# Optimization experiments

Measured on AMD Instinct MI355X. Metric: run time of the kernel, lower is better.

## Reference

```python
import jax, jax.numpy as jnp
import numpy as np
from jax import lax


def setup_inputs() -> dict:
    key = jax.random.key(0)
    k1, k2 = jax.random.split(key)
    N, dim, m = 8192, 1024, 1024
    x = jax.random.normal(k1, (N, dim), dtype=jnp.float32)
    vectors = jax.random.normal(k2, (m, dim), dtype=jnp.float32) * 0.01
    bias = jnp.zeros((dim,), dtype=jnp.float32)
    return {"x": x, "vectors": vectors, "bias": bias}


def reference(x, vectors, bias):
    # Normalize each reflection vector to unit length: [m, d]
    v_normed = vectors / jnp.linalg.norm(vectors, axis=1, keepdims=True)

    def step(out, v):
        # out: [N, d], v: [d]
        proj = out @ v                       # [N]
        out = out - 2.0 * proj[:, None] * v  # rank-1 Householder update
        return out, None

    out, _ = lax.scan(step, x, v_normed)
    return out + bias
```

## Files before the change

### kernel.cpp

```cpp
#include <hip/hip_runtime.h>
#include <hip/hip_bf16.h>

typedef __attribute__((ext_vector_type(8))) short short8;
typedef __attribute__((ext_vector_type(4))) short s16x4;
typedef __attribute__((ext_vector_type(4))) float f32x4;

static __device__ inline short f2bf(float f) {
    unsigned u = __float_as_uint(f);
    unsigned r = (u + 0x7fffu + ((u >> 16) & 1u)) >> 16;
    return (short)r;
}
static __device__ inline float bf2f(short h) {
    return __uint_as_float(((unsigned)(unsigned short)h) << 16);
}

static __device__ inline int swz32(int row, int slot) {
    return row * 32 + ((slot ^ ((row >> 1) & 3)) << 3);
}
static __device__ inline int swz64(int row, int slot) {
    return row * 64 + ((slot ^ (row & 7)) << 3);
}

__global__ __launch_bounds__(256) void k_prep(const float* __restrict__ vec,
                                              short* __restrict__ Vh, short* __restrict__ Vl,
                                              short* __restrict__ Vth, short* __restrict__ Vtl,
                                              int m, int dim) {
    __shared__ float ps[32][9];
    __shared__ float invs[32];
    __shared__ float tile[32][33];
    int r0 = blockIdx.x * 32;
    int t = threadIdx.x;
    int r = t >> 3, seg = t & 7;
    const float* src = vec + (size_t)(r0 + r) * dim + seg * 128;
    float ss = 0.f;
#pragma unroll 8
    for (int i = 0; i < 32; ++i) {
        float4 v = *(const float4*)&src[i * 4];
        ss += v.x * v.x + v.y * v.y + v.z * v.z + v.w * v.w;
    }
    ps[r][seg] = ss;
    __syncthreads();
    if (t < 32) {
        float s = 0.f;
#pragma unroll
        for (int q = 0; q < 8; ++q) s += ps[t][q];
        invs[t] = 1.0f / sqrtf(s);
    }
    __syncthreads();
    float inv = invs[r];
    int c4 = (t & 7) * 4;
    for (int ct = 0; ct < dim / 32; ++ct) {
        float4 v = *(const float4*)&vec[(size_t)(r0 + r) * dim + ct * 32 + c4];
        float f[4] = {v.x * inv, v.y * inv, v.z * inv, v.w * inv};
        s16x4 h, l;
#pragma unroll
        for (int q = 0; q < 4; ++q) {
            h[q] = f2bf(f[q]);
            l[q] = f2bf(f[q] - bf2f(h[q]));
            tile[r][c4 + q] = f[q];
        }
        *(s16x4*)&Vh[(size_t)(r0 + r) * dim + ct * 32 + c4] = h;
        *(s16x4*)&Vl[(size_t)(r0 + r) * dim + ct * 32 + c4] = l;
        __syncthreads();
        s16x4 th, tl;
#pragma unroll
        for (int q = 0; q < 4; ++q) {
            float ff = tile[c4 + q][r];
            th[q] = f2bf(ff);
            tl[q] = f2bf(ff - bf2f(th[q]));
        }
        *(s16x4*)&Vth[(size_t)(ct * 32 + r) * m + r0 + c4] = th;
        *(s16x4*)&Vtl[(size_t)(ct * 32 + r) * m + r0 + c4] = tl;
        __syncthreads();
    }
}

__global__ __launch_bounds__(256) void k_cast(const float* __restrict__ X,
                                              short* __restrict__ Xh, int n4) {
    for (int i = blockIdx.x * blockDim.x + threadIdx.x; i < n4; i += gridDim.x * blockDim.x) {
        float4 v = ((const float4*)X)[i];
        float f[4] = {v.x, v.y, v.z, v.w};
        s16x4 h;
#pragma unroll
        for (int q = 0; q < 4; ++q) h[q] = f2bf(f[q]);
        *(s16x4*)&Xh[(size_t)i * 4] = h;
    }
}

template<int MODE, int TRI>
__global__ __launch_bounds__(256) void k_nt64g(
    const short* __restrict__ Ah, const short* __restrict__ Al,
    const short* __restrict__ Bh, const short* __restrict__ Bl,
    float* __restrict__ Cf, short* __restrict__ Ch, short* __restrict__ Cl,
    int K, int lda, int ldb, int ldc) {
    __shared__ short As[2][2][64 * 32];
    __shared__ short Bs[2][2][64 * 32];
    int i0 = blockIdx.y * 64, j0 = blockIdx.x * 64;
    if (TRI == 2 && j0 < i0) return;
    int KE = (TRI == 1) ? (j0 + 64) : K;
    int t = threadIdx.x, lane = t & 63, wave = t >> 6;
    int wr = wave >> 1, wc = wave & 1;
    int srow = wave * 16 + (lane >> 2);
    int sslot = (lane & 3) ^ ((lane >> 3) & 3);
    const short* gAh = &Ah[(size_t)(i0 + srow) * lda + sslot * 8];
    const short* gAl = &Al[(size_t)(i0 + srow) * lda + sslot * 8];
    const short* gBh = &Bh[(size_t)(j0 + srow) * ldb + sslot * 8];
    const short* gBl = &Bl[(size_t)(j0 + srow) * ldb + sslot * 8];
    auto stage = [&](int buf, int k0) {
        __builtin_amdgcn_global_load_lds((const __attribute__((address_space(1))) void*)&gAh[k0],
            (__attribute__((address_space(3))) void*)&As[buf][0][wave * 512], 16, 0, 0);
        __builtin_amdgcn_global_load_lds((const __attribute__((address_space(1))) void*)&gAl[k0],
            (__attribute__((address_space(3))) void*)&As[buf][1][wave * 512], 16, 0, 0);
        __builtin_amdgcn_global_load_lds((const __attribute__((address_space(1))) void*)&gBh[k0],
            (__attribute__((address_space(3))) void*)&Bs[buf][0][wave * 512], 16, 0, 0);
        __builtin_amdgcn_global_load_lds((const __attribute__((address_space(1))) void*)&gBl[k0],
            (__attribute__((address_space(3))) void*)&Bs[buf][1][wave * 512], 16, 0, 0);
    };
    int nIter = KE >> 5;
    stage(0, 0);
    f32x4 acc[2][2] = {};
    for (int it = 0; it < nIter; ++it) {
        int c = it & 1;
        if (it + 1 < nIter) {
            stage(c ^ 1, (it + 1) << 5);
            asm volatile("s_waitcnt vmcnt(4)" ::: "memory");
        } else {
            asm volatile("s_waitcnt vmcnt(0)" ::: "memory");
        }
        __builtin_amdgcn_s_barrier();
        __builtin_amdgcn_sched_barrier(0);
        int g = lane >> 4;
        short8 ah[2], al2[2], bh[2], bl2[2];
#pragma unroll
        for (int i = 0; i < 2; ++i) {
            int ro = swz32(wr * 32 + i * 16 + (lane & 15), g);
            ah[i] = *(const short8*)&As[c][0][ro];
            al2[i] = *(const short8*)&As[c][1][ro];
        }
#pragma unroll
        for (int j = 0; j < 2; ++j) {
            int ro = swz32(wc * 32 + j * 16 + (lane & 15), g);
            bh[j] = *(const short8*)&Bs[c][0][ro];
            bl2[j] = *(const short8*)&Bs[c][1][ro];
        }
#pragma unroll
        for (int i = 0; i < 2; ++i)
#pragma unroll
            for (int j = 0; j < 2; ++j) {
                acc[i][j] = __builtin_amdgcn_mfma_f32_16x16x32_bf16(ah[i], bh[j], acc[i][j], 0, 0, 0);
                acc[i][j] = __builtin_amdgcn_mfma_f32_16x16x32_bf16(ah[i], bl2[j], acc[i][j], 0, 0, 0);
                acc[i][j] = __builtin_amdgcn_mfma_f32_16x16x32_bf16(al2[i], bh[j], acc[i][j], 0, 0, 0);
            }
        asm volatile("s_waitcnt lgkmcnt(0)" ::: "memory");
        __builtin_amdgcn_s_barrier();
    }
#pragma unroll
    for (int i = 0; i < 2; ++i)
#pragma unroll
        for (int j = 0; j < 2; ++j) {
            int row0 = i0 + wr * 32 + i * 16 + ((lane >> 4) << 2);
            int col = j0 + wc * 32 + j * 16 + (lane & 15);
#pragma unroll
            for (int r = 0; r < 4; ++r) {
                float v = acc[i][j][r];
                size_t idx = (size_t)(row0 + r) * ldc + col;
                if (MODE == 2) {
                    Ch[idx] = f2bf((((row0 + r) == col) ? 1.f : 0.f) - v);
                } else {
                    short h = f2bf(v);
                    short l = f2bf(v - bf2f(h));
                    Ch[idx] = h;
                    Cl[idx] = l;
                    if (MODE == 3) Cf[idx] = v;
                }
            }
        }
}

__global__ __launch_bounds__(256) void k_baseinv2(const float* __restrict__ G,
                                                  short* __restrict__ Th, short* __restrict__ Tl,
                                                  short* __restrict__ Tth, short* __restrict__ Ttl,
                                                  int m) {
    __shared__ float Rs[64 * 64];
    int d = blockIdx.x >> 4, g = blockIdx.x & 15;
    int b0 = d * 64;
    int t = threadIdx.x, lane = t & 63, wave = t >> 6;
    {
        int r = t >> 2, c00 = (t & 3) * 16;
#pragma unroll
        for (int q = 0; q < 4; ++q)
            *(float4*)&Rs[r * 64 + c00 + q * 4] =
                *(const float4*)&G[(size_t)(b0 + r) * m + b0 + c00 + q * 4];
    }
    __syncthreads();
    int c = g * 4 + wave;
    float x = 0.f;
    for (int r = c; r >= 0; --r) {
        float prod = Rs[r * 64 + lane] * x;
        float s = prod;
#pragma unroll
        for (int off = 32; off; off >>= 1) s += __shfl_xor(s, off, 64);
        if (lane == r) x = ((r == c) ? 2.f : 0.f) - 2.f * s;
    }
    short h = f2bf(x);
    short l = f2bf(x - bf2f(h));
    Th[(size_t)(b0 + lane) * m + b0 + c] = h;
    Tl[(size_t)(b0 + lane) * m + b0 + c] = l;
    Tth[(size_t)(b0 + c) * m + b0 + lane] = h;
    Ttl[(size_t)(b0 + c) * m + b0 + lane] = l;
}

__global__ __launch_bounds__(256) void k_tree64f(const float* __restrict__ G,
                                                 short* __restrict__ Th, short* __restrict__ Tl,
                                                 short* __restrict__ Tth, short* __restrict__ Ttl,
                                                 int m) {
    __shared__ float Gb[64 * 65];
    __shared__ float Ai[64 * 65];
    __shared__ float Ci[64 * 64];
    __shared__ float Tm[64 * 64];
    int p = blockIdx.x;
    int a0 = p * 128, c0 = a0 + 64;
    int t = threadIdx.x;
    {
        int r = t >> 2, c00 = (t & 3) * 16;
#pragma unroll
        for (int q = 0; q < 4; ++q) {
            *(float4*)&Gb[r * 65 + c00 + q * 4] =
                *(const float4*)&G[(size_t)(a0 + r) * m + c0 + c00 + q * 4];
            s16x4 ha = *(const s16x4*)&Th[(size_t)(a0 + r) * m + a0 + c00 + q * 4];
            s16x4 la = *(const s16x4*)&Tl[(size_t)(a0 + r) * m + a0 + c00 + q * 4];
            s16x4 hc = *(const s16x4*)&Th[(size_t)(c0 + r) * m + c0 + c00 + q * 4];
            s16x4 lc = *(const s16x4*)&Tl[(size_t)(c0 + r) * m + c0 + c00 + q * 4];
#pragma unroll
            for (int e = 0; e < 4; ++e) {
                Ai[r * 65 + c00 + q * 4 + e] = bf2f(ha[e]) + bf2f(la[e]);
                Ci[r * 64 + c00 + q * 4 + e] = bf2f(hc[e]) + bf2f(lc[e]);
            }
        }
    }
    __syncthreads();
    int tx = t & 15, ty = t >> 4;
    float acc[4][4] = {};
#pragma unroll 4
    for (int k = 0; k < 64; ++k) {
        float av[4], bv[4];
#pragma unroll
        for (int i = 0; i < 4; ++i) av[i] = Gb[(ty * 4 + i) * 65 + k];
#pragma unroll
        for (int j = 0; j < 4; ++j) bv[j] = Ci[k * 64 + tx * 4 + j];
#pragma unroll
        for (int i = 0; i < 4; ++i)
#pragma unroll
            for (int j = 0; j < 4; ++j) acc[i][j] += av[i] * bv[j];
    }
#pragma unroll
    for (int i = 0; i < 4; ++i)
#pragma unroll
        for (int j = 0; j < 4; ++j) Tm[(ty * 4 + i) * 64 + tx * 4 + j] = acc[i][j];
    __syncthreads();
    float acc2[4][4] = {};
#pragma unroll 4
    for (int k = 0; k < 64; ++k) {
        float av[4], bv[4];
#pragma unroll
        for (int i = 0; i < 4; ++i) av[i] = Ai[(ty * 4 + i) * 65 + k];
#pragma unroll
        for (int j = 0; j < 4; ++j) bv[j] = Tm[k * 64 + tx * 4 + j];
#pragma unroll
        for (int i = 0; i < 4; ++i)
#pragma unroll
            for (int j = 0; j < 4; ++j) acc2[i][j] += av[i] * bv[j];
    }
#pragma unroll
    for (int i = 0; i < 4; ++i)
#pragma unroll
        for (int j = 0; j < 4; ++j) {
            float v = -acc2[i][j];
            short h = f2bf(v);
            short l = f2bf(v - bf2f(h));
            int R = a0 + ty * 4 + i, C = c0 + tx * 4 + j;
            Th[(size_t)R * m + C] = h;
            Tl[(size_t)R * m + C] = l;
            Tth[(size_t)C * m + R] = h;
            Ttl[(size_t)C * m + R] = l;
        }
}

template<int PHASE>
__global__ __launch_bounds__(256) void k_trimm(
    const short* __restrict__ Ah, const short* __restrict__ Al,
    const short* __restrict__ Bh, const short* __restrict__ Bl,
    short* __restrict__ C1h, short* __restrict__ C1l,
    short* __restrict__ C2h, short* __restrict__ C2l,
    int m, int s) {
    __shared__ short As[2][64 * 32];
    __shared__ short Bs[2][64 * 32];
    int p = blockIdx.z;
    int a0 = 2 * p * s, c0 = a0 + s;
    int r0 = blockIdx.y * 64, ct = blockIdx.x * 64;
    int KS = (PHASE == 1) ? 0 : r0;
    int KE = (PHASE == 1) ? (ct + 64) : s;
    size_t tbase = (size_t)p * s * s;
    int t = threadIdx.x, lane = t & 63, wave = t >> 6;
    int wr = wave >> 1, wc = wave & 1;
    int srow = t >> 2, slot = t & 3;
    int sofs = swz32(srow, slot);
    int gofs = slot * 8;
    f32x4 acc[2][2] = {};
    for (int k0 = KS; k0 < KE; k0 += 32) {
        __syncthreads();
        if (PHASE == 1) {
            *(short8*)&As[0][sofs] = *(const short8*)&Ah[(size_t)(a0 + r0 + srow) * m + c0 + k0 + gofs];
            *(short8*)&As[1][sofs] = *(const short8*)&Al[(size_t)(a0 + r0 + srow) * m + c0 + k0 + gofs];
            *(short8*)&Bs[0][sofs] = *(const short8*)&Bh[(size_t)(c0 + ct + srow) * m + c0 + k0 + gofs];
            *(short8*)&Bs[1][sofs] = *(const short8*)&Bl[(size_t)(c0 + ct + srow) * m + c0 + k0 + gofs];
        } else {
            *(short8*)&As[0][sofs] = *(const short8*)&Ah[(size_t)(a0 + r0 + srow) * m + a0 + k0 + gofs];
            *(short8*)&As[1][sofs] = *(const short8*)&Al[(size_t)(a0 + r0 + srow) * m + a0 + k0 + gofs];
            *(short8*)&Bs[0][sofs] = *(const short8*)&Bh[tbase + (size_t)(ct + srow) * s + k0 + gofs];
            *(short8*)&Bs[1][sofs] = *(const short8*)&Bl[tbase + (size_t)(ct + srow) * s + k0 + gofs];
        }
        __syncthreads();
        int g = lane >> 4;
        short8 ah[2], al2[2], bh[2], bl2[2];
#pragma unroll
        for (int i = 0; i < 2; ++i) {
            int ro = swz32(wr * 32 + i * 16 + (lane & 15), g);
            ah[i] = *(const short8*)&As[0][ro];
            al2[i] = *(const short8*)&As[1][ro];
        }
#pragma unroll
        for (int j = 0; j < 2; ++j) {
            int ro = swz32(wc * 32 + j * 16 + (lane & 15), g);
            bh[j] = *(const short8*)&Bs[0][ro];
            bl2[j] = *(const short8*)&Bs[1][ro];
        }
#pragma unroll
        for (int i = 0; i < 2; ++i)
#pragma unroll
            for (int j = 0; j < 2; ++j) {
                acc[i][j] = __builtin_amdgcn_mfma_f32_16x16x32_bf16(ah[i], bh[j], acc[i][j], 0, 0, 0);
                acc[i][j] = __builtin_amdgcn_mfma_f32_16x16x32_bf16(ah[i], bl2[j], acc[i][j], 0, 0, 0);
                acc[i][j] = __builtin_amdgcn_mfma_f32_16x16x32_bf16(al2[i], bh[j], acc[i][j], 0, 0, 0);
            }
    }
#pragma unroll
    for (int i = 0; i < 2; ++i)
#pragma unroll
        for (int j = 0; j < 2; ++j) {
            int row0 = r0 + wr * 32 + i * 16 + ((lane >> 4) << 2);
            int col = ct + wc * 32 + j * 16 + (lane & 15);
#pragma unroll
            for (int r = 0; r < 4; ++r) {
                if (PHASE == 1) {
                    float v = acc[i][j][r];
                    short h = f2bf(v);
                    short l = f2bf(v - bf2f(h));
                    size_t idx = tbase + (size_t)col * s + row0 + r;
                    C1h[idx] = h;
                    C1l[idx] = l;
                } else {
                    float v = -acc[i][j][r];
                    short h = f2bf(v);
                    short l = f2bf(v - bf2f(h));
                    int R = a0 + row0 + r, Cc = c0 + col;
                    C1h[(size_t)R * m + Cc] = h;
                    C1l[(size_t)R * m + Cc] = l;
                    C2h[(size_t)Cc * m + R] = h;
                    C2l[(size_t)Cc * m + R] = l;
                }
            }
        }
}

__global__ __launch_bounds__(256) void k_apply4(const short* __restrict__ xh,
                                                const short* __restrict__ Qt,
                                                const float* __restrict__ bias,
                                                float* __restrict__ out, int dim) {
    __shared__ short As[2][128 * 64];
    __shared__ short Bs[2][128 * 64];
    int nwg = gridDim.x * gridDim.y;
    int flat = blockIdx.y * gridDim.x + blockIdx.x;
    int cpx = nwg >> 3;
    int L = (flat & 7) * cpx + (flat >> 3);
    int m0 = (L / gridDim.x) * 128, n0 = (L % gridDim.x) * 128;
    int t = threadIdx.x, lane = t & 63, wave = t >> 6;
    int wr = wave >> 1, wc = wave & 1;
    int sr = lane >> 3;
    int sslot = (lane & 7) ^ (sr & 7);
    auto stage = [&](int buf, int k0) {
#pragma unroll
        for (int q = 0; q < 4; ++q) {
            int rg = wave * 4 + q;
            int row = rg * 8 + sr;
            const short* gA = &xh[(size_t)(m0 + row) * dim + k0 + sslot * 8];
            const short* gB = &Qt[(size_t)(n0 + row) * dim + k0 + sslot * 8];
            __builtin_amdgcn_global_load_lds(
                (const __attribute__((address_space(1))) void*)gA,
                (__attribute__((address_space(3))) void*)&As[buf][rg * 8 * 64], 16, 0, 0);
            __builtin_amdgcn_global_load_lds(
                (const __attribute__((address_space(1))) void*)gB,
                (__attribute__((address_space(3))) void*)&Bs[buf][rg * 8 * 64], 16, 0, 0);
        }
    };
    int nIter = dim >> 6;
    stage(0, 0);
    f32x4 acc[4][4] = {};
    for (int it = 0; it < nIter; ++it) {
        int c = it & 1;
        if (it + 1 < nIter) {
            stage(c ^ 1, (it + 1) << 6);
            asm volatile("s_waitcnt vmcnt(8)" ::: "memory");
        } else {
            asm volatile("s_waitcnt vmcnt(0)" ::: "memory");
        }
        __builtin_amdgcn_s_barrier();
        __builtin_amdgcn_sched_barrier(0);
#pragma unroll
        for (int kk = 0; kk < 2; ++kk) {
            int g = kk * 4 + (lane >> 4);
            short8 af[4], bf_[4];
#pragma unroll
            for (int i = 0; i < 4; ++i)
                af[i] = *(const short8*)&As[c][swz64(wr * 64 + i * 16 + (lane & 15), g)];
#pragma unroll
            for (int j = 0; j < 4; ++j)
                bf_[j] = *(const short8*)&Bs[c][swz64(wc * 64 + j * 16 + (lane & 15), g)];
#pragma unroll
            for (int i = 0; i < 4; ++i)
#pragma unroll
                for (int j = 0; j < 4; ++j)
                    acc[i][j] = __builtin_amdgcn_mfma_f32_16x16x32_bf16(af[i], bf_[j], acc[i][j], 0, 0, 0);
        }
        asm volatile("s_waitcnt lgkmcnt(0)" ::: "memory");
        __builtin_amdgcn_s_barrier();
    }
#pragma unroll
    for (int i = 0; i < 4; ++i)
#pragma unroll
        for (int j = 0; j < 4; ++j) {
            int row = m0 + wr * 64 + i * 16 + (lane >> 4) * 4;
            int col = n0 + wc * 64 + j * 16 + (lane & 15);
            float b = bias[col];
#pragma unroll
            for (int r = 0; r < 4; ++r)
                out[(size_t)(row + r) * dim + col] = acc[i][j][r] + b;
        }
}

extern "C" void kernel_launch(void* const* d_in, const int* in_sizes, int n_in,
                              void* d_out, int out_size, void* d_ws, size_t ws_size,
                              hipStream_t stream) {
    const float* x = (const float*)d_in[0];
    const float* vec = (const float*)d_in[1];
    const float* bias = (const float*)d_in[2];
    float* out = (float*)d_out;

    int dim = in_sizes[2];
    int m = in_sizes[1] / dim;
    int n = in_sizes[0] / dim;

    const size_t MD = (size_t)m * dim;
    const size_t MM = (size_t)m * m;

    char* cur = (char*)d_ws;
    auto alloc_f = [&](size_t nelem) { float* p = (float*)cur; cur += nelem * 4; return p; };
    auto alloc_s = [&](size_t nelem) { short* p = (short*)cur; cur += nelem * 2; return p; };
    float* G   = alloc_f(MM);
    short* Vh  = alloc_s(MD);
    short* Vl  = alloc_s(MD);
    short* Vth = alloc_s(MD);
    short* Vtl = alloc_s(MD);
    short* Gh  = alloc_s(MM);
    short* Gl  = alloc_s(MM);
    short* Th  = alloc_s(MM);
    short* Tl  = alloc_s(MM);
    short* Tth = alloc_s(MM);
    short* Ttl = alloc_s(MM);
    short* Wh  = alloc_s(MD);
    short* Wl  = alloc_s(MD);
    short* Qt  = alloc_s((size_t)dim * dim);
    short* tmph = alloc_s(MM / 2);
    short* tmpl = alloc_s(MM / 2);
    short* xh  = alloc_s((size_t)n * dim);

    k_prep<<<m / 32, 256, 0, stream>>>(vec, Vh, Vl, Vth, Vtl, m, dim);

    k_nt64g<3, 2><<<dim3(m / 64, m / 64), 256, 0, stream>>>(Vh, Vl, Vh, Vl, G, Gh, Gl,
                                                            dim, dim, dim, m);
    k_baseinv2<<<(m / 64) * 16, 256, 0, stream>>>(G, Th, Tl, Tth, Ttl, m);
    k_tree64f<<<m / 128, 256, 0, stream>>>(G, Th, Tl, Tth, Ttl, m);
    for (int s = 128; s < m; s <<= 1) {
        dim3 g(s / 64, s / 64, m / (2 * s));
        k_trimm<1><<<g, 256, 0, stream>>>(Gh, Gl, Tth, Ttl, tmph, tmpl, nullptr, nullptr, m, s);
        k_trimm<2><<<g, 256, 0, stream>>>(Th, Tl, tmph, tmpl, Th, Tl, Tth, Ttl, m, s);
    }

    k_nt64g<1, 1><<<dim3(m / 64, dim / 64), 256, 0, stream>>>(Vth, Vtl, Tth, Ttl, nullptr, Wh, Wl,
                                                              m, m, m, m);
    k_nt64g<2, 0><<<dim3(dim / 64, dim / 64), 256, 0, stream>>>(Vth, Vtl, Wh, Wl, nullptr, Qt, nullptr,
                                                                m, m, m, dim);

    k_cast<<<2048, 256, 0, stream>>>(x, xh, (int)((size_t)n * dim / 4));
    k_apply4<<<dim3(dim / 128, n / 128), 256, 0, stream>>>(xh, Qt, bias, out, dim);
}
```

Baseline: 187.4 us.

## Split vector prep into norm and transpose kernels; switch GEMM staging to register prefetch

Vector normalization is split into a per-row norm kernel and a 2D-grid cast/transpose kernel. The old prep used only m/32 blocks, each looping serially over all columns, so this exposes more parallelism. The small compact-WY GEMMs move from direct global-to-LDS async loads to register-prefetched loads with one __syncthreads per iteration. The final apply GEMM drops its K tile from 64 to 32, halving LDS use at the cost of twice as many barrier iterations. These are several independent changes, and the apply-kernel change could cost time on the dominant GEMM.

```diff
diff --git a/kernel.cpp b/kernel.cpp
--- a/kernel.cpp
+++ b/kernel.cpp
@@ -17,62 +17,54 @@
 static __device__ inline int swz32(int row, int slot) {
     return row * 32 + ((slot ^ ((row >> 1) & 3)) << 3);
 }
-static __device__ inline int swz64(int row, int slot) {
-    return row * 64 + ((slot ^ (row & 7)) << 3);
-}
-
-__global__ __launch_bounds__(256) void k_prep(const float* __restrict__ vec,
-                                              short* __restrict__ Vh, short* __restrict__ Vl,
-                                              short* __restrict__ Vth, short* __restrict__ Vtl,
-                                              int m, int dim) {
-    __shared__ float ps[32][9];
-    __shared__ float invs[32];
+
+__global__ __launch_bounds__(256) void k_norms(const float* __restrict__ vec,
+                                               float* __restrict__ inv, int dim) {
+    int row = blockIdx.x * 4 + (threadIdx.x >> 6);
+    int lane = threadIdx.x & 63;
+    const float4* src = (const float4*)(vec + (size_t)row * dim);
+    float ss = 0.f;
+#pragma unroll
+    for (int i = 0; i < 4; ++i) {
+        float4 v = src[lane + 64 * i];
+        ss += v.x * v.x + v.y * v.y + v.z * v.z + v.w * v.w;
+    }
+#pragma unroll
+    for (int off = 32; off; off >>= 1) ss += __shfl_xor(ss, off, 64);
+    if (lane == 0) inv[row] = 1.0f / sqrtf(ss);
+}
+
+__global__ __launch_bounds__(256) void k_prep2(const float* __restrict__ vec,
+                                               const float* __restrict__ inv,
+                                               short* __restrict__ Vh, short* __restrict__ Vl,
+                                               short* __restrict__ Vth, short* __restrict__ Vtl,
+                                               int m, int dim) {
     __shared__ float tile[32][33];
-    int r0 = blockIdx.x * 32;
+    int c0 = blockIdx.x * 32, r0 = blockIdx.y * 32;
     int t = threadIdx.x;
-    int r = t >> 3, seg = t & 7;
-    const float* src = vec + (size_t)(r0 + r) * dim + seg * 128;
-    float ss = 0.f;
-#pragma unroll 8
-    for (int i = 0; i < 32; ++i) {
-        float4 v = *(const float4*)&src[i * 4];
-        ss += v.x * v.x + v.y * v.y + v.z * v.z + v.w * v.w;
-    }
-    ps[r][seg] = ss;
+    int r = t >> 3, c4 = (t & 7) * 4;
+    float iv = inv[r0 + r];
+    float4 v = *(const float4*)&vec[(size_t)(r0 + r) * dim + c0 + c4];
+    float f[4] = {v.x * iv, v.y * iv, v.z * iv, v.w * iv};
+    s16x4 h, l;
+#pragma unroll
+    for (int q = 0; q < 4; ++q) {
+        h[q] = f2bf(f[q]);
+        l[q] = f2bf(f[q] - bf2f(h[q]));
+        tile[r][c4 + q] = f[q];
+    }
+    *(s16x4*)&Vh[(size_t)(r0 + r) * dim + c0 + c4] = h;
+    *(s16x4*)&Vl[(size_t)(r0 + r) * dim + c0 + c4] = l;
     __syncthreads();
-    if (t < 32) {
-        float s = 0.f;
-#pragma unroll
-        for (int q = 0; q < 8; ++q) s += ps[t][q];
-        invs[t] = 1.0f / sqrtf(s);
-    }
-    __syncthreads();
-    float inv = invs[r];
-    int c4 = (t & 7) * 4;
-    for (int ct = 0; ct < dim / 32; ++ct) {
-        float4 v = *(const float4*)&vec[(size_t)(r0 + r) * dim + ct * 32 + c4];
-        float f[4] = {v.x * inv, v.y * inv, v.z * inv, v.w * inv};
-        s16x4 h, l;
-#pragma unroll
-        for (int q = 0; q < 4; ++q) {
-            h[q] = f2bf(f[q]);
-            l[q] = f2bf(f[q] - bf2f(h[q]));
-            tile[r][c4 + q] = f[q];
-        }
-        *(s16x4*)&Vh[(size_t)(r0 + r) * dim + ct * 32 + c4] = h;
-        *(s16x4*)&Vl[(size_t)(r0 + r) * dim + ct * 32 + c4] = l;
-        __syncthreads();
-        s16x4 th, tl;
-#pragma unroll
-        for (int q = 0; q < 4; ++q) {
-            float ff = tile[c4 + q][r];
-            th[q] = f2bf(ff);
-            tl[q] = f2bf(ff - bf2f(th[q]));
-        }
-        *(s16x4*)&Vth[(size_t)(ct * 32 + r) * m + r0 + c4] = th;
-        *(s16x4*)&Vtl[(size_t)(ct * 32 + r) * m + r0 + c4] = tl;
-        __syncthreads();
-    }
+    s16x4 th, tl;
+#pragma unroll
+    for (int q = 0; q < 4; ++q) {
+        float ff = tile[c4 + q][r];
+        th[q] = f2bf(ff);
+        tl[q] = f2bf(ff - bf2f(th[q]));
+    }
+    *(s16x4*)&Vth[(size_t)(c0 + r) * m + r0 + c4] = th;
+    *(s16x4*)&Vtl[(size_t)(c0 + r) * m + r0 + c4] = tl;
 }
 
 __global__ __launch_bounds__(256) void k_cast(const float* __restrict__ X,
@@ -88,7 +80,7 @@
 }
 
 template<int MODE, int TRI>
-__global__ __launch_bounds__(256) void k_nt64g(
+__global__ __launch_bounds__(256) void k_nt64p(
     const short* __restrict__ Ah, const short* __restrict__ Al,
     const short* __restrict__ Bh, const short* __restrict__ Bl,
     float* __restrict__ Cf, short* __restrict__ Ch, short* __restrict__ Cl,
@@ -100,48 +92,47 @@
     int KE = (TRI == 1) ? (j0 + 64) : K;
     int t = threadIdx.x, lane = t & 63, wave = t >> 6;
     int wr = wave >> 1, wc = wave & 1;
-    int srow = wave * 16 + (lane >> 2);
-    int sslot = (lane & 3) ^ ((lane >> 3) & 3);
-    const short* gAh = &Ah[(size_t)(i0 + srow) * lda + sslot * 8];
-    const short* gAl = &Al[(size_t)(i0 + srow) * lda + sslot * 8];
-    const short* gBh = &Bh[(size_t)(j0 + srow) * ldb + sslot * 8];
-    const short* gBl = &Bl[(size_t)(j0 + srow) * ldb + sslot * 8];
-    auto stage = [&](int buf, int k0) {
-        __builtin_amdgcn_global_load_lds((const __attribute__((address_space(1))) void*)&gAh[k0],
-            (__attribute__((address_space(3))) void*)&As[buf][0][wave * 512], 16, 0, 0);
-        __builtin_amdgcn_global_load_lds((const __attribute__((address_space(1))) void*)&gAl[k0],
-            (__attribute__((address_space(3))) void*)&As[buf][1][wave * 512], 16, 0, 0);
-        __builtin_amdgcn_global_load_lds((const __attribute__((address_space(1))) void*)&gBh[k0],
-            (__attribute__((address_space(3))) void*)&Bs[buf][0][wave * 512], 16, 0, 0);
-        __builtin_amdgcn_global_load_lds((const __attribute__((address_space(1))) void*)&gBl[k0],
-            (__attribute__((address_space(3))) void*)&Bs[buf][1][wave * 512], 16, 0, 0);
-    };
+    int srow = t >> 2, slot = t & 3;
+    int sofs = swz32(srow, slot);
+    int gofs = slot * 8;
+    const short* gA_h = &Ah[(size_t)(i0 + srow) * lda + gofs];
+    const short* gA_l = &Al[(size_t)(i0 + srow) * lda + gofs];
+    const short* gB_h = &Bh[(size_t)(j0 + srow) * ldb + gofs];
+    const short* gB_l = &Bl[(size_t)(j0 + srow) * ldb + gofs];
+    short8 pAh = *(const short8*)&gA_h[0];
+    short8 pAl = *(const short8*)&gA_l[0];
+    short8 pBh = *(const short8*)&gB_h[0];
+    short8 pBl = *(const short8*)&gB_l[0];
+    *(short8*)&As[0][0][sofs] = pAh;
+    *(short8*)&As[0][1][sofs] = pAl;
+    *(short8*)&Bs[0][0][sofs] = pBh;
+    *(short8*)&Bs[0][1][sofs] = pBl;
+    f32x4 acc[2][2] = {};
     int nIter = KE >> 5;
-    stage(0, 0);
-    f32x4 acc[2][2] = {};
+    int cur = 0;
     for (int it = 0; it < nIter; ++it) {
-        int c = it & 1;
-        if (it + 1 < nIter) {
-            stage(c ^ 1, (it + 1) << 5);
-            asm volatile("s_waitcnt vmcnt(4)" ::: "memory");
-        } else {
-            asm volatile("s_waitcnt vmcnt(0)" ::: "memory");
-        }
-        __builtin_amdgcn_s_barrier();
-        __builtin_amdgcn_sched_barrier(0);
+        __syncthreads();
+        int kn = (it + 1) << 5;
+        bool have = kn < KE;
+        if (have) {
+            pAh = *(const short8*)&gA_h[kn];
+            pAl = *(const short8*)&gA_l[kn];
+            pBh = *(const short8*)&gB_h[kn];
+            pBl = *(const short8*)&gB_l[kn];
+        }
         int g = lane >> 4;
         short8 ah[2], al2[2], bh[2], bl2[2];
 #pragma unroll
         for (int i = 0; i < 2; ++i) {
             int ro = swz32(wr * 32 + i * 16 + (lane & 15), g);
-            ah[i] = *(const short8*)&As[c][0][ro];
-            al2[i] = *(const short8*)&As[c][1][ro];
+            ah[i] = *(const short8*)&As[cur][0][ro];
+            al2[i] = *(const short8*)&As[cur][1][ro];
         }
 #pragma unroll
         for (int j = 0; j < 2; ++j) {
             int ro = swz32(wc * 32 + j * 16 + (lane & 15), g);
-            bh[j] = *(const short8*)&Bs[c][0][ro];
-            bl2[j] = *(const short8*)&Bs[c][1][ro];
+            bh[j] = *(const short8*)&Bs[cur][0][ro];
+            bl2[j] = *(const short8*)&Bs[cur][1][ro];
         }
 #pragma unroll
         for (int i = 0; i < 2; ++i)
@@ -151,8 +142,13 @@
                 acc[i][j] = __builtin_amdgcn_mfma_f32_16x16x32_bf16(ah[i], bl2[j], acc[i][j], 0, 0, 0);
                 acc[i][j] = __builtin_amdgcn_mfma_f32_16x16x32_bf16(al2[i], bh[j], acc[i][j], 0, 0, 0);
             }
-        asm volatile("s_waitcnt lgkmcnt(0)" ::: "memory");
-        __builtin_amdgcn_s_barrier();
+        if (have) {
+            *(short8*)&As[cur ^ 1][0][sofs] = pAh;
+            *(short8*)&As[cur ^ 1][1][sofs] = pAl;
+            *(short8*)&Bs[cur ^ 1][0][sofs] = pBh;
+            *(short8*)&Bs[cur ^ 1][1][sofs] = pBl;
+        }
+        cur ^= 1;
     }
 #pragma unroll
     for (int i = 0; i < 2; ++i)
@@ -373,12 +369,12 @@
         }
 }
 
-__global__ __launch_bounds__(256) void k_apply4(const short* __restrict__ xh,
+__global__ __launch_bounds__(256) void k_apply5(const short* __restrict__ xh,
                                                 const short* __restrict__ Qt,
                                                 const float* __restrict__ bias,
                                                 float* __restrict__ out, int dim) {
-    __shared__ short As[2][128 * 64];
-    __shared__ short Bs[2][128 * 64];
+    __shared__ short As[2][128 * 32];
+    __shared__ short Bs[2][128 * 32];
     int nwg = gridDim.x * gridDim.y;
     int flat = blockIdx.y * gridDim.x + blockIdx.x;
     int cpx = nwg >> 3;
@@ -386,52 +382,49 @@
     int m0 = (L / gridDim.x) * 128, n0 = (L % gridDim.x) * 128;
     int t = threadIdx.x, lane = t & 63, wave = t >> 6;
     int wr = wave >> 1, wc = wave & 1;
-    int sr = lane >> 3;
-    int sslot = (lane & 7) ^ (sr & 7);
+    int srIn = lane >> 2;
+    int sslot = (lane & 3) ^ ((lane >> 3) & 3);
     auto stage = [&](int buf, int k0) {
 #pragma unroll
-        for (int q = 0; q < 4; ++q) {
-            int rg = wave * 4 + q;
-            int row = rg * 8 + sr;
+        for (int q = 0; q < 2; ++q) {
+            int rg = wave * 2 + q;
+            int row = rg * 16 + srIn;
             const short* gA = &xh[(size_t)(m0 + row) * dim + k0 + sslot * 8];
             const short* gB = &Qt[(size_t)(n0 + row) * dim + k0 + sslot * 8];
             __builtin_amdgcn_global_load_lds(
                 (const __attribute__((address_space(1))) void*)gA,
-                (__attribute__((address_space(3))) void*)&As[buf][rg * 8 * 64], 16, 0, 0);
+                (__attribute__((address_space(3))) void*)&As[buf][rg * 16 * 32], 16, 0, 0);
             __builtin_amdgcn_global_load_lds(
                 (const __attribute__((address_space(1))) void*)gB,
-                (__attribute__((address_space(3))) void*)&Bs[buf][rg * 8 * 64], 16, 0, 0);
+                (__attribute__((address_space(3))) void*)&Bs[buf][rg * 16 * 32], 16, 0, 0);
         }
     };
-    int nIter = dim >> 6;
+    int nIter = dim >> 5;
     stage(0, 0);
     f32x4 acc[4][4] = {};
     for (int it = 0; it < nIter; ++it) {
         int c = it & 1;
         if (it + 1 < nIter) {
-            stage(c ^ 1, (it + 1) << 6);
-            asm volatile("s_waitcnt vmcnt(8)" ::: "memory");
+            stage(c ^ 1, (it + 1) << 5);
+            asm volatile("s_waitcnt vmcnt(4)" ::: "memory");
         } else {
             asm volatile("s_waitcnt vmcnt(0)" ::: "memory");
         }
         __builtin_amdgcn_s_barrier();
         __builtin_amdgcn_sched_barrier(0);
-#pragma unroll
-        for (int kk = 0; kk < 2; ++kk) {
-            int g = kk * 4 + (lane >> 4);
-            short8 af[4], bf_[4];
-#pragma unroll
-            for (int i = 0; i < 4; ++i)
-                af[i] = *(const short8*)&As[c][swz64(wr * 64 + i * 16 + (lane & 15), g)];
+        int g = lane >> 4;
+        short8 af[4], bf_[4];
+#pragma unroll
+        for (int i = 0; i < 4; ++i)
+            af[i] = *(const short8*)&As[c][swz32(wr * 64 + i * 16 + (lane & 15), g)];
+#pragma unroll
+        for (int j = 0; j < 4; ++j)
+            bf_[j] = *(const short8*)&Bs[c][swz32(wc * 64 + j * 16 + (lane & 15), g)];
+#pragma unroll
+        for (int i = 0; i < 4; ++i)
 #pragma unroll
             for (int j = 0; j < 4; ++j)
-                bf_[j] = *(const short8*)&Bs[c][swz64(wc * 64 + j * 16 + (lane & 15), g)];
-#pragma unroll
-            for (int i = 0; i < 4; ++i)
-#pragma unroll
-                for (int j = 0; j < 4; ++j)
-                    acc[i][j] = __builtin_amdgcn_mfma_f32_16x16x32_bf16(af[i], bf_[j], acc[i][j], 0, 0, 0);
-        }
+                acc[i][j] = __builtin_amdgcn_mfma_f32_16x16x32_bf16(af[i], bf_[j], acc[i][j], 0, 0, 0);
         asm volatile("s_waitcnt lgkmcnt(0)" ::: "memory");
         __builtin_amdgcn_s_barrier();
     }
@@ -466,7 +459,8 @@
     char* cur = (char*)d_ws;
     auto alloc_f = [&](size_t nelem) { float* p = (float*)cur; cur += nelem * 4; return p; };
     auto alloc_s = [&](size_t nelem) { short* p = (short*)cur; cur += nelem * 2; return p; };
-    float* G   = alloc_f(MM);
+    float* G    = alloc_f(MM);
+    float* invn = alloc_f(m);
     short* Vh  = alloc_s(MD);
     short* Vl  = alloc_s(MD);
     short* Vth = alloc_s(MD);
@@ -484,9 +478,10 @@
     short* tmpl = alloc_s(MM / 2);
     short* xh  = alloc_s((size_t)n * dim);
 
-    k_prep<<<m / 32, 256, 0, stream>>>(vec, Vh, Vl, Vth, Vtl, m, dim);
-
-    k_nt64g<3, 2><<<dim3(m / 64, m / 64), 256, 0, stream>>>(Vh, Vl, Vh, Vl, G, Gh, Gl,
+    k_norms<<<m / 4, 256, 0, stream>>>(vec, invn, dim);
+    k_prep2<<<dim3(dim / 32, m / 32), 256, 0, stream>>>(vec, invn, Vh, Vl, Vth, Vtl, m, dim);
+
+    k_nt64p<3, 2><<<dim3(m / 64, m / 64), 256, 0, stream>>>(Vh, Vl, Vh, Vl, G, Gh, Gl,
                                                             dim, dim, dim, m);
     k_baseinv2<<<(m / 64) * 16, 256, 0, stream>>>(G, Th, Tl, Tth, Ttl, m);
     k_tree64f<<<m / 128, 256, 0, stream>>>(G, Th, Tl, Tth, Ttl, m);
@@ -496,11 +491,11 @@
         k_trimm<2><<<g, 256, 0, stream>>>(Th, Tl, tmph, tmpl, Th, Tl, Tth, Ttl, m, s);
     }
 
-    k_nt64g<1, 1><<<dim3(m / 64, dim / 64), 256, 0, stream>>>(Vth, Vtl, Tth, Ttl, nullptr, Wh, Wl,
+    k_nt64p<1, 1><<<dim3(m / 64, dim / 64), 256, 0, stream>>>(Vth, Vtl, Tth, Ttl, nullptr, Wh, Wl,
                                                               m, m, m, m);
-    k_nt64g<2, 0><<<dim3(dim / 64, dim / 64), 256, 0, stream>>>(Vth, Vtl, Wh, Wl, nullptr, Qt, nullptr,
+    k_nt64p<2, 0><<<dim3(dim / 64, dim / 64), 256, 0, stream>>>(Vth, Vtl, Wh, Wl, nullptr, Qt, nullptr,
                                                                 m, m, m, dim);
 
     k_cast<<<2048, 256, 0, stream>>>(x, xh, (int)((size_t)n * dim / 4));
-    k_apply4<<<dim3(dim / 128, n / 128), 256, 0, stream>>>(xh, Qt, bias, out, dim);
-}
+    k_apply5<<<dim3(dim / 128, n / 128), 256, 0, stream>>>(xh, Qt, bias, out, dim);
+}
```

After: 171.8 us. 1.09x faster.
